# Optimization experiments

Hardware: AMD Instinct MI355X
Metric: run time of the kernel (lower is better)

Reference implementation:

```python
import jax, jax.numpy as jnp
import numpy as np

B, N, C_IN = 8, 2048, 2


def _pdist(x):
    # (B,N,N) pairwise euclidean distances
    d2 = jnp.sum((x[:, :, None, :] - x[:, None, :, :]) ** 2, axis=-1)
    return jnp.sqrt(d2)


def _knn_idx(x, k):
    d = _pdist(x)
    return jnp.argsort(d, axis=-1)[:, :, :k]  # includes self (dist 0)


def _ball_idx(x, radius, nsample):
    # deterministic ball query: neighbors with dist<=radius in ascending index
    # order, cyclically repeated if fewer than nsample (self is always in ball)
    d = _pdist(x)
    n = x.shape[1]
    mask = d <= radius
    ar = jnp.arange(n)
    order = jnp.argsort(jnp.where(mask, ar, ar + n), axis=-1)  # valid idx first
    count = jnp.sum(mask, axis=-1, keepdims=True)               # >= 1
    pos = jnp.arange(nsample)[None, None, :] % count            # (B,N,nsample)
    return jnp.take_along_axis(order, pos, axis=-1)


def _gather(x, idx):
    # x: (B,N,C), idx: (B,N,S) -> (B,N,S,C)
    return jax.vmap(lambda pts, ind: pts[ind])(x, idx)


def _mlp2(f, w0, b0, w1, b1):
    # 1x1 Conv2D stack == per-neighbor dense + relu
    f = jnp.maximum(jnp.einsum('bnsc,cd->bnsd', f, w0) + b0, 0.0)
    f = jnp.maximum(jnp.einsum('bnsc,cd->bnsd', f, w1) + b1, 0.0)
    return f


def _dense_relu(x, w, b):
    return jnp.maximum(x @ w + b, 0.0)


def _forward(x,
             sa1_w0, sa1_b0, sa1_w1, sa1_b1,
             sa2_w0, sa2_b0, sa2_w1, sa2_b1,
             sa3_w0, sa3_b0, sa3_w1, sa3_b1,
             fp1_w0, fp1_b0, fp1_w1, fp1_b1,
             fp2_w0, fp2_b0, fp2_w1, fp2_b1,
             fc1_w, fc1_b, fc2_w, fc2_b, out_w, out_b):
    # SA1: knn(k=32) on raw points, mlps [64,64], mean over neighbors
    x1 = jnp.mean(_mlp2(_gather(x, _knn_idx(x, 32)), sa1_w0, sa1_b0, sa1_w1, sa1_b1), axis=2)
    # SA2: ball query radius=0.2, nsample=32, mlps [128,128]
    x2 = jnp.mean(_mlp2(_gather(x1, _ball_idx(x1, 0.2, 32)), sa2_w0, sa2_b0, sa2_w1, sa2_b1), axis=2)
    # SA3: ball query radius=0.4, nsample=64, mlps [256,256]
    x3 = jnp.mean(_mlp2(_gather(x2, _ball_idx(x2, 0.4, 64)), sa3_w0, sa3_b0, sa3_w1, sa3_b1), axis=2)
    # FP1: dense mlps on local (x2), concat global (x3)
    h = _dense_relu(_dense_relu(x2, fp1_w0, fp1_b0), fp1_w1, fp1_b1)
    h = jnp.concatenate([h, x3], axis=-1)
    # FP2: dense mlps on local (x1), concat previous
    g = _dense_relu(_dense_relu(x1, fp2_w0, fp2_b0), fp2_w1, fp2_b1)
    g = jnp.concatenate([g, h], axis=-1)
    g = _dense_relu(g, fc1_w, fc1_b)
    g = _dense_relu(g, fc2_w, fc2_b)
    return jax.nn.sigmoid(g @ out_w + out_b)  # (B,N,1)


def setup_inputs() -> dict:
    key = jax.random.key(0)
    ks = iter(jax.random.split(key, 40))
    def w(i, o):
        return (jax.random.normal(next(ks), (i, o), jnp.float32) / np.sqrt(i)).astype(jnp.float32)
    def b(o):
        return jnp.zeros((o,), jnp.float32)
    inp = {
        'x': jax.random.normal(next(ks), (B, N, C_IN), jnp.float32),
        'sa1_w0': w(2, 64),   'sa1_b0': b(64),  'sa1_w1': w(64, 64),   'sa1_b1': b(64),
        'sa2_w0': w(64, 128), 'sa2_b0': b(128), 'sa2_w1': w(128, 128), 'sa2_b1': b(128),
        'sa3_w0': w(128, 256),'sa3_b0': b(256), 'sa3_w1': w(256, 256), 'sa3_b1': b(256),
        'fp1_w0': w(128, 512),'fp1_b0': b(512), 'fp1_w1': w(512, 512), 'fp1_b1': b(512),
        'fp2_w0': w(64, 256), 'fp2_b0': b(256), 'fp2_w1': w(256, 256), 'fp2_b1': b(256),
        'fc1_w': w(1024, 256),'fc1_b': b(256),
        'fc2_w': w(256, 128), 'fc2_b': b(128),
        'out_w': w(128, 1),   'out_b': b(1),
    }
    return inp


def reference(x,
              sa1_w0, sa1_b0, sa1_w1, sa1_b1,
              sa2_w0, sa2_b0, sa2_w1, sa2_b1,
              sa3_w0, sa3_b0, sa3_w1, sa3_b1,
              fp1_w0, fp1_b0, fp1_w1, fp1_b1,
              fp2_w0, fp2_b0, fp2_w1, fp2_b1,
              fc1_w, fc1_b, fc2_w, fc2_b, out_w, out_b):
    return _forward(x,
                    sa1_w0, sa1_b0, sa1_w1, sa1_b1,
                    sa2_w0, sa2_b0, sa2_w1, sa2_b1,
                    sa3_w0, sa3_b0, sa3_w1, sa3_b1,
                    fp1_w0, fp1_b0, fp1_w1, fp1_b1,
                    fp2_w0, fp2_b0, fp2_w1, fp2_b1,
                    fc1_w, fc1_b, fc2_w, fc2_b, out_w, out_b)
```

## Files before the change

### kernel.cpp

```cpp
#include <hip/hip_runtime.h>
#include <hip/hip_bf16.h>
#include <cstdint>

#define M_ROWS 16384

typedef __attribute__((ext_vector_type(8))) short short8;
typedef __attribute__((ext_vector_type(4))) float f32x4;

__device__ __forceinline__ unsigned long long umin64(unsigned long long a,
                                                     unsigned long long b) {
  return a < b ? a : b;
}

__global__ __launch_bounds__(256) void gemm_bias_relu(
    const float* __restrict__ X, int ldx,
    const float* __restrict__ W,
    const float* __restrict__ bias,
    float* __restrict__ Y, int ldy,
    int N, int K)
{
  __shared__ __align__(16) float As[16][68];
  __shared__ __align__(16) float Bs[16][68];
  int tid = threadIdx.x;
  int tx = tid & 15, ty = tid >> 4;
  int m0 = blockIdx.y << 6, n0 = blockIdx.x << 6;
  float acc[4][4] = {};
  for (int k0 = 0; k0 < K; k0 += 16) {
#pragma unroll
    for (int i = 0; i < 4; i++) {
      int idx = tid + (i << 8);
      int m = idx >> 4, k = idx & 15;
      As[k][m] = (k0 + k < K) ? X[(size_t)(m0 + m) * ldx + k0 + k] : 0.f;
    }
#pragma unroll
    for (int i = 0; i < 4; i++) {
      int idx = tid + (i << 8);
      int n = idx & 63, k = idx >> 6;
      Bs[k][n] = (k0 + k < K) ? W[(size_t)(k0 + k) * N + n0 + n] : 0.f;
    }
    __syncthreads();
#pragma unroll
    for (int k = 0; k < 16; k++) {
      float4 a4 = *(const float4*)&As[k][ty << 2];
      float4 b4 = *(const float4*)&Bs[k][tx << 2];
      float av[4] = {a4.x, a4.y, a4.z, a4.w};
      float bv[4] = {b4.x, b4.y, b4.z, b4.w};
#pragma unroll
      for (int i = 0; i < 4; i++)
#pragma unroll
        for (int j = 0; j < 4; j++)
          acc[i][j] += av[i] * bv[j];
    }
    __syncthreads();
  }
  float4 bb = *(const float4*)&bias[n0 + (tx << 2)];
  float bv[4] = {bb.x, bb.y, bb.z, bb.w};
#pragma unroll
  for (int i = 0; i < 4; i++) {
    int m = m0 + (ty << 2) + i;
    float4 o;
    o.x = fmaxf(acc[i][0] + bv[0], 0.f);
    o.y = fmaxf(acc[i][1] + bv[1], 0.f);
    o.z = fmaxf(acc[i][2] + bv[2], 0.f);
    o.w = fmaxf(acc[i][3] + bv[3], 0.f);
    *(float4*)&Y[(size_t)m * ldy + n0 + (tx << 2)] = o;
  }
}

struct TJobs {
  const float* W[8];
  __hip_bfloat16* Wt[8];
  int K[8], N[8], bx[8], off[8];
};

__global__ __launch_bounds__(256) void transpose_cast_all(TJobs jb)
{
  __shared__ float tile[32][33];
  int bid = blockIdx.x;
  int j = 0;
#pragma unroll
  for (int t = 1; t < 8; t++)
    if (bid >= jb.off[t]) j = t;
  int rel = bid - jb.off[j];
  int K = jb.K[j], N = jb.N[j];
  const float* W = jb.W[j];
  __hip_bfloat16* Wt = jb.Wt[j];
  int n0 = (rel % jb.bx[j]) << 5, k0 = (rel / jb.bx[j]) << 5;
  int c = threadIdx.x & 31, i0 = threadIdx.x >> 5;
#pragma unroll
  for (int p = 0; p < 4; p++) {
    int i = i0 + p * 8;
    tile[i][c] = W[(size_t)(k0 + i) * N + n0 + c];
  }
  __syncthreads();
#pragma unroll
  for (int p = 0; p < 4; p++) {
    int r = i0 + p * 8;
    Wt[(size_t)(n0 + r) * K + k0 + c] = (__hip_bfloat16)tile[c][r];
  }
}

template <bool OUT_BF16>
__global__ __launch_bounds__(256) void gemm_mfma(
    const __hip_bfloat16* __restrict__ A, int lda,
    const __hip_bfloat16* __restrict__ Wt, int ldw,
    const float* __restrict__ bias,
    void* __restrict__ Y, int ldy, int N, int K)
{
  __shared__ __align__(16) short As[128][40];
  __shared__ __align__(16) short Bs[128][40];
  int tid = threadIdx.x;
  int wave = tid >> 6, lane = tid & 63;
  int quad = lane >> 4, l16 = lane & 15;
  int m0 = blockIdx.y << 7, n0 = blockIdx.x << 7;
  int wm = (wave >> 1) << 6, wn = (wave & 1) << 6;
  f32x4 acc[4][4] = {};
  const short* Ag = (const short*)A;
  const short* Bg = (const short*)Wt;
  int srow = tid >> 2, sq = tid & 3;
  for (int k0 = 0; k0 < K; k0 += 32) {
#pragma unroll
    for (int h = 0; h < 2; h++) {
      int r = srow + (h << 6);
      uint4 va = *(const uint4*)&Ag[(size_t)(m0 + r) * lda + k0 + sq * 8];
      *(uint4*)&As[r][sq * 8] = va;
      uint4 vb = *(const uint4*)&Bg[(size_t)(n0 + r) * ldw + k0 + sq * 8];
      *(uint4*)&Bs[r][sq * 8] = vb;
    }
    __syncthreads();
    short8 a[4], b[4];
#pragma unroll
    for (int mi = 0; mi < 4; mi++)
      a[mi] = *(const short8*)&As[wm + mi * 16 + l16][quad * 8];
#pragma unroll
    for (int ni = 0; ni < 4; ni++)
      b[ni] = *(const short8*)&Bs[wn + ni * 16 + l16][quad * 8];
#pragma unroll
    for (int mi = 0; mi < 4; mi++)
#pragma unroll
      for (int ni = 0; ni < 4; ni++)
        acc[mi][ni] = __builtin_amdgcn_mfma_f32_16x16x32_bf16(
            a[mi], b[ni], acc[mi][ni], 0, 0, 0);
    __syncthreads();
  }
  float bn[4];
#pragma unroll
  for (int ni = 0; ni < 4; ni++) bn[ni] = bias[n0 + wn + ni * 16 + l16];
#pragma unroll
  for (int mi = 0; mi < 4; mi++)
#pragma unroll
    for (int ni = 0; ni < 4; ni++) {
      int n = n0 + wn + ni * 16 + l16;
#pragma unroll
      for (int r = 0; r < 4; r++) {
        int m = m0 + wm + mi * 16 + quad * 4 + r;
        float v = fmaxf(acc[mi][ni][r] + bn[ni], 0.f);
        if (OUT_BF16)
          ((__hip_bfloat16*)Y)[(size_t)m * ldy + n] = (__hip_bfloat16)v;
        else
          ((float*)Y)[(size_t)m * ldy + n] = v;
      }
    }
}

struct GJobs {
  const short* A[3];
  const short* W[3];
  const float* bias[3];
  __hip_bfloat16* Y[3];
  int lda[3], ldw[3], ldy[3], N[3], K[3], xt[3], off[3];
};

__global__ __launch_bounds__(256) void gemm_mfma_multi(GJobs g)
{
  __shared__ __align__(16) short As[128][40];
  __shared__ __align__(16) short Bs[128][40];
  int bid = blockIdx.x;
  int j = 0;
#pragma unroll
  for (int t = 1; t < 3; t++)
    if (bid >= g.off[t]) j = t;
  int rel = bid - g.off[j];
  int xt = g.xt[j];
  int m0 = (rel / xt) << 7, n0 = (rel % xt) << 7;
  int lda = g.lda[j], ldw = g.ldw[j], ldy = g.ldy[j], K = g.K[j];
  const short* Ag = g.A[j];
  const short* Bg = g.W[j];
  const float* bias = g.bias[j];
  __hip_bfloat16* Y = g.Y[j];

  int tid = threadIdx.x;
  int wave = tid >> 6, lane = tid & 63;
  int quad = lane >> 4, l16 = lane & 15;
  int wm = (wave >> 1) << 6, wn = (wave & 1) << 6;
  f32x4 acc[4][4] = {};
  int srow = tid >> 2, sq = tid & 3;
  for (int k0 = 0; k0 < K; k0 += 32) {
#pragma unroll
    for (int h = 0; h < 2; h++) {
      int r = srow + (h << 6);
      uint4 va = *(const uint4*)&Ag[(size_t)(m0 + r) * lda + k0 + sq * 8];
      *(uint4*)&As[r][sq * 8] = va;
      uint4 vb = *(const uint4*)&Bg[(size_t)(n0 + r) * ldw + k0 + sq * 8];
      *(uint4*)&Bs[r][sq * 8] = vb;
    }
    __syncthreads();
    short8 a[4], b[4];
#pragma unroll
    for (int mi = 0; mi < 4; mi++)
      a[mi] = *(const short8*)&As[wm + mi * 16 + l16][quad * 8];
#pragma unroll
    for (int ni = 0; ni < 4; ni++)
      b[ni] = *(const short8*)&Bs[wn + ni * 16 + l16][quad * 8];
#pragma unroll
    for (int mi = 0; mi < 4; mi++)
#pragma unroll
      for (int ni = 0; ni < 4; ni++)
        acc[mi][ni] = __builtin_amdgcn_mfma_f32_16x16x32_bf16(
            a[mi], b[ni], acc[mi][ni], 0, 0, 0);
    __syncthreads();
  }
  float bn[4];
#pragma unroll
  for (int ni = 0; ni < 4; ni++) bn[ni] = bias[n0 + wn + ni * 16 + l16];
#pragma unroll
  for (int mi = 0; mi < 4; mi++)
#pragma unroll
    for (int ni = 0; ni < 4; ni++) {
      int n = n0 + wn + ni * 16 + l16;
#pragma unroll
      for (int r = 0; r < 4; r++) {
        int m = m0 + wm + mi * 16 + quad * 4 + r;
        float v = fmaxf(acc[mi][ni][r] + bn[ni], 0.f);
        Y[(size_t)m * ldy + n] = (__hip_bfloat16)v;
      }
    }
}

__global__ __launch_bounds__(256) void gemm_fc2_out(
    const __hip_bfloat16* __restrict__ A,
    const __hip_bfloat16* __restrict__ Wt,
    const float* __restrict__ bias,
    const float* __restrict__ wout,
    const float* __restrict__ bout,
    float* __restrict__ out)
{
  __shared__ __align__(16) short As[128][40];
  __shared__ __align__(16) short Bs[128][40];
  __shared__ float red[128][2];
  const int N = 128, K = 256, lda = 256, ldw = 256;
  int tid = threadIdx.x;
  int wave = tid >> 6, lane = tid & 63;
  int quad = lane >> 4, l16 = lane & 15;
  int m0 = blockIdx.y << 7;
  int wm = (wave >> 1) << 6, wn = (wave & 1) << 6;
  f32x4 acc[4][4] = {};
  const short* Ag = (const short*)A;
  const short* Bg = (const short*)Wt;
  int srow = tid >> 2, sq = tid & 3;
  for (int k0 = 0; k0 < K; k0 += 32) {
#pragma unroll
    for (int h = 0; h < 2; h++) {
      int r = srow + (h << 6);
      uint4 va = *(const uint4*)&Ag[(size_t)(m0 + r) * lda + k0 + sq * 8];
      *(uint4*)&As[r][sq * 8] = va;
      uint4 vb = *(const uint4*)&Bg[(size_t)(r % N) * ldw + k0 + sq * 8];
      *(uint4*)&Bs[r][sq * 8] = vb;
    }
    __syncthreads();
    short8 a[4], b[4];
#pragma unroll
    for (int mi = 0; mi < 4; mi++)
      a[mi] = *(const short8*)&As[wm + mi * 16 + l16][quad * 8];
#pragma unroll
    for (int ni = 0; ni < 4; ni++)
      b[ni] = *(const short8*)&Bs[wn + ni * 16 + l16][quad * 8];
#pragma unroll
    for (int mi = 0; mi < 4; mi++)
#pragma unroll
      for (int ni = 0; ni < 4; ni++)
        acc[mi][ni] = __builtin_amdgcn_mfma_f32_16x16x32_bf16(
            a[mi], b[ni], acc[mi][ni], 0, 0, 0);
    __syncthreads();
  }
  float bn[4], wo[4];
#pragma unroll
  for (int ni = 0; ni < 4; ni++) {
    int n = wn + ni * 16 + l16;
    bn[ni] = bias[n];
    wo[ni] = wout[n];
  }
  float sacc[4][4];
#pragma unroll
  for (int mi = 0; mi < 4; mi++)
#pragma unroll
    for (int r = 0; r < 4; r++) {
      float s = 0.f;
#pragma unroll
      for (int ni = 0; ni < 4; ni++)
        s += fmaxf(acc[mi][ni][r] + bn[ni], 0.f) * wo[ni];
      sacc[mi][r] = s;
    }
#pragma unroll
  for (int off = 1; off < 16; off <<= 1)
#pragma unroll
    for (int mi = 0; mi < 4; mi++)
#pragma unroll
      for (int r = 0; r < 4; r++)
        sacc[mi][r] += __shfl_xor(sacc[mi][r], off);
  int wp = wave & 1;
  if (l16 == 0) {
#pragma unroll
    for (int mi = 0; mi < 4; mi++)
#pragma unroll
      for (int r = 0; r < 4; r++)
        red[wm + mi * 16 + quad * 4 + r][wp] = sacc[mi][r];
  }
  __syncthreads();
  if (tid < 128) {
    float s = red[tid][0] + red[tid][1] + bout[0];
    out[(size_t)(m0 + tid)] = 1.f / (1.f + expf(-s));
  }
}

__global__ __launch_bounds__(256) void knn_mean_kernel(
    const float* __restrict__ X,
    const float* __restrict__ G1,
    float* __restrict__ X1,
    __hip_bfloat16* __restrict__ X1b,
    __hip_bfloat16* __restrict__ X1lo,
    float* __restrict__ nrmX1)
{
  int q = blockIdx.x;
  int base = q & ~2047;
  int tid = threadIdx.x;
  __shared__ unsigned long long lmins[256];
  __shared__ unsigned long long qmins[64];
  __shared__ unsigned long long surv[2048];
  __shared__ unsigned long long thr;
  __shared__ int scnt;
  __shared__ int selidx[32];
  if (tid == 0) scnt = 0;
  float qx = X[(size_t)q * 2], qy = X[(size_t)q * 2 + 1];
  unsigned long long key[8];
#pragma unroll
  for (int u = 0; u < 8; u++) {
    int j = (u << 8) + tid;
    float dx = X[(size_t)(base + j) * 2] - qx;
    float dy = X[(size_t)(base + j) * 2 + 1] - qy;
    float d2 = dx * dx + dy * dy;
    key[u] = ((unsigned long long)__float_as_uint(d2) << 32) | (unsigned)j;
  }
  unsigned long long lm = key[0];
#pragma unroll
  for (int u = 1; u < 8; u++) lm = umin64(lm, key[u]);
  lmins[tid] = lm;
  __syncthreads();
  if (tid < 64) {
    unsigned long long qm = umin64(umin64(lmins[tid], lmins[tid + 64]),
                                   umin64(lmins[tid + 128], lmins[tid + 192]));
    qmins[tid] = qm;
    int rank = 0;
    for (int i = 0; i < 64; i++) rank += (qmins[i] < qm);
    if (rank == 31) thr = qm;
  }
  __syncthreads();
  unsigned long long T = thr;
#pragma unroll
  for (int u = 0; u < 8; u++) {
    if (key[u] <= T) {
      int p = atomicAdd(&scnt, 1);
      surv[p] = key[u];
    }
  }
  __syncthreads();
  int s = scnt;
  for (int i = tid; i < s; i += 256) {
    unsigned long long c = surv[i];
    int r = 0;
    for (int j2 = 0; j2 < s; j2++) r += (surv[j2] < c);
    if (r < 32) selidx[r] = (int)(c & 0xffffffffULL);
  }
  __syncthreads();
  if (tid < 64) {
    float acc = 0.f;
#pragma unroll 4
    for (int sI = 0; sI < 32; sI++)
      acc += G1[(size_t)(base + selidx[sI]) * 64 + tid];
    float v = acc * (1.0f / 32.0f);
    X1[(size_t)q * 64 + tid] = v;
    __hip_bfloat16 hi = (__hip_bfloat16)v;
    X1b[(size_t)q * 64 + tid] = hi;
    X1lo[(size_t)q * 64 + tid] = (__hip_bfloat16)(v - (float)hi);
    float nv = v * v;
#pragma unroll
    for (int off = 32; off > 0; off >>= 1) nv += __shfl_down(nv, off);
    if (tid == 0) nrmX1[q] = nv;
  }
}

template <int C>
__global__ __launch_bounds__(256) void ball_mask_mfma(
    const float* __restrict__ F32,
    const __hip_bfloat16* __restrict__ Fhi,
    const __hip_bfloat16* __restrict__ Flo,
    const float* __restrict__ nrm,
    unsigned long long* __restrict__ mask,
    float r2)
{
  __shared__ __align__(16) short Qh[128][40];
  __shared__ __align__(16) short Ql[128][40];
  __shared__ __align__(16) short Ch[128][40];
  __shared__ __align__(16) short Cl[128][40];
  __shared__ unsigned int tw[128][4];
  __shared__ float nqs[128], ncs[128];
  int tid = threadIdx.x;
  int p = blockIdx.x;
  int qt = 0;
  while (p >= 16 - qt) { p -= 16 - qt; qt++; }
  int ct = qt + p;
  int b0 = blockIdx.y << 11;
  int q0 = b0 + (qt << 7), c0 = b0 + (ct << 7);
  tw[tid >> 1][(tid & 1) * 2] = 0;
  tw[tid >> 1][(tid & 1) * 2 + 1] = 0;
  if (tid < 128) nqs[tid] = nrm[q0 + tid];
  else ncs[tid - 128] = nrm[c0 + tid - 128];

  int wave = tid >> 6, lane = tid & 63;
  int quad = lane >> 4, l16 = lane & 15;
  int wm = (wave >> 1) << 6, wn = (wave & 1) << 6;
  f32x4 acc[4][4] = {};
  const short* QH = (const short*)Fhi;
  const short* QL = (const short*)Flo;
  int srow = tid >> 2, sq = tid & 3;
  for (int k0 = 0; k0 < C; k0 += 32) {
#pragma unroll
    for (int h = 0; h < 2; h++) {
      int r = srow + (h << 6);
      *(uint4*)&Qh[r][sq * 8] = *(const uint4*)&QH[(size_t)(q0 + r) * C + k0 + sq * 8];
      *(uint4*)&Ql[r][sq * 8] = *(const uint4*)&QL[(size_t)(q0 + r) * C + k0 + sq * 8];
      *(uint4*)&Ch[r][sq * 8] = *(const uint4*)&QH[(size_t)(c0 + r) * C + k0 + sq * 8];
      *(uint4*)&Cl[r][sq * 8] = *(const uint4*)&QL[(size_t)(c0 + r) * C + k0 + sq * 8];
    }
    __syncthreads();
    short8 ah[4], al[4];
#pragma unroll
    for (int mi = 0; mi < 4; mi++) {
      ah[mi] = *(const short8*)&Qh[wm + mi * 16 + l16][quad * 8];
      al[mi] = *(const short8*)&Ql[wm + mi * 16 + l16][quad * 8];
    }
#pragma unroll
    for (int ni = 0; ni < 4; ni++) {
      short8 bh = *(const short8*)&Ch[wn + ni * 16 + l16][quad * 8];
      short8 bl = *(const short8*)&Cl[wn + ni * 16 + l16][quad * 8];
#pragma unroll
      for (int mi = 0; mi < 4; mi++) {
        acc[mi][ni] = __builtin_amdgcn_mfma_f32_16x16x32_bf16(ah[mi], bh, acc[mi][ni], 0, 0, 0);
        acc[mi][ni] = __builtin_amdgcn_mfma_f32_16x16x32_bf16(ah[mi], bl, acc[mi][ni], 0, 0, 0);
        acc[mi][ni] = __builtin_amdgcn_mfma_f32_16x16x32_bf16(al[mi], bh, acc[mi][ni], 0, 0, 0);
      }
    }
    __syncthreads();
  }
  unsigned long long memb = 0, fb = 0;
#pragma unroll
  for (int mi = 0; mi < 4; mi++)
#pragma unroll
    for (int ni = 0; ni < 4; ni++)
#pragma unroll
      for (int r = 0; r < 4; r++) {
        int e = (mi << 4) | (ni << 2) | r;
        float nqv = nqs[wm + mi * 16 + quad * 4 + r];
        float ncv = ncs[wn + ni * 16 + l16];
        float d2a = nqv + ncv - 2.f * acc[mi][ni][r];
        float eps = 4.0e-5f * (nqv + ncv) + 1.0e-6f;
        if (d2a < r2 - eps) memb |= 1ull << e;
        else if (d2a <= r2 + eps) fb |= 1ull << e;
      }
  while (fb) {
    int e = __builtin_ctzll(fb);
    fb &= fb - 1;
    int mi = e >> 4, ni = (e >> 2) & 3, r = e & 3;
    int qrow = q0 + wm + mi * 16 + quad * 4 + r;
    int ccol = c0 + wn + ni * 16 + l16;
    float a2 = 0.f;
    for (int k = 0; k < C; k++) {
      float d = F32[(size_t)qrow * C + k] - F32[(size_t)ccol * C + k];
      a2 = fmaf(d, d, a2);
    }
    if (a2 <= r2) memb |= 1ull << e;
  }
#pragma unroll
  for (int ni = 0; ni < 4; ni++) {
    int cl = wn + ni * 16 + l16;
    unsigned int w0b = 0, w1b = 0;
#pragma unroll
    for (int mi = 0; mi < 4; mi++)
#pragma unroll
      for (int r = 0; r < 4; r++)
        if (memb & (1ull << ((mi << 4) | (ni << 2) | r))) {
          unsigned int bitpos = ((mi & 1) << 4) | (quad << 2) | r;
          if (mi < 2) w0b |= 1u << bitpos;
          else w1b |= 1u << bitpos;
        }
    if (w0b) atomicOr(&tw[cl][(wm >> 5)], w0b);
    if (w1b) atomicOr(&tw[cl][(wm >> 5) + 1], w1b);
  }
  __syncthreads();
  {
    int row = tid >> 1, half = tid & 1;
    int wq = row >> 5, sb = row & 31;
    unsigned int lo = 0, hi = 0;
    for (int j = 0; j < 32; j++) {
      lo |= ((tw[half * 64 + j][wq] >> sb) & 1u) << j;
      hi |= ((tw[half * 64 + 32 + j][wq] >> sb) & 1u) << j;
    }
    mask[(size_t)(q0 + row) * 32 + (ct << 1) + half] =
        ((unsigned long long)hi << 32) | lo;
  }
  if (qt != ct) {
    int row = tid >> 1, word = tid & 1;
    unsigned long long v = (unsigned long long)tw[row][word * 2] |
                           ((unsigned long long)tw[row][word * 2 + 1] << 32);
    mask[(size_t)(c0 + row) * 32 + (qt << 1) + word] = v;
  }
}

template <typename TIn>
__global__ void ball_gather_kernel(
    const unsigned long long* __restrict__ mask,
    const TIn* __restrict__ H, int CH,
    float* __restrict__ Yf, __hip_bfloat16* __restrict__ Yb,
    __hip_bfloat16* __restrict__ Ylo, float* __restrict__ nrm,
    int ldy, int S)
{
  int q = blockIdx.x;
  int base = q & ~2047;
  int tid = threadIdx.x;
  __shared__ int idxl[64];
  __shared__ float wtab[64];
  __shared__ float npart[4];
  __shared__ int scount;
  if (tid < 32) {
    unsigned long long w = mask[(size_t)q * 32 + tid];
    int cnt = __popcll(w);
    int inc = cnt;
#pragma unroll
    for (int off = 1; off < 32; off <<= 1) {
      int o = __shfl_up(inc, off);
      if (tid >= off) inc += o;
    }
    if (tid == 31) scount = inc;
    int p = inc - cnt;
    while (w && p < 64) {
      int j = (tid << 6) + __builtin_ctzll(w);
      w &= w - 1;
      idxl[p++] = j;
    }
  }
  __syncthreads();
  int c = scount;
  if (tid < 64) {
    int p = tid;
    int cnt = (p < c && p < S) ? ((S - 1 - p) / c + 1) : 0;
    wtab[p] = (float)cnt / (float)S;
  }
  __syncthreads();
  float acc = 0.f;
  int lim = c < S ? c : S;
#pragma unroll 4
  for (int s = 0; s < lim; s++)
    acc += wtab[s] * (float)H[(size_t)(base + idxl[s]) * CH + tid];
  if (Yf) Yf[(size_t)q * ldy + tid] = acc;
  if (Yb) Yb[(size_t)q * ldy + tid] = (__hip_bfloat16)acc;
  if (Ylo) {
    __hip_bfloat16 hi = (__hip_bfloat16)acc;
    Ylo[(size_t)q * ldy + tid] = (__hip_bfloat16)(acc - (float)hi);
  }
  if (nrm) {
    float nv = acc * acc;
#pragma unroll
    for (int off = 32; off > 0; off >>= 1) nv += __shfl_down(nv, off);
    if ((tid & 63) == 0) npart[tid >> 6] = nv;
    __syncthreads();
    if (tid == 0) {
      float t = 0.f;
      for (int w = 0; w < (blockDim.x >> 6); w++) t += npart[w];
      nrm[q] = t;
    }
  }
}

extern "C" void kernel_launch(void* const* d_in, const int* in_sizes, int n_in,
                              void* d_out, int out_size, void* d_ws,
                              size_t ws_size, hipStream_t stream)
{
  const float* x      = (const float*)d_in[0];
  const float* sa1_w0 = (const float*)d_in[1];
  const float* sa1_b0 = (const float*)d_in[2];
  const float* sa1_w1 = (const float*)d_in[3];
  const float* sa1_b1 = (const float*)d_in[4];
  const float* sa2_w0 = (const float*)d_in[5];
  const float* sa2_b0 = (const float*)d_in[6];
  const float* sa2_w1 = (const float*)d_in[7];
  const float* sa2_b1 = (const float*)d_in[8];
  const float* sa3_w0 = (const float*)d_in[9];
  const float* sa3_b0 = (const float*)d_in[10];
  const float* sa3_w1 = (const float*)d_in[11];
  const float* sa3_b1 = (const float*)d_in[12];
  const float* fp1_w0 = (const float*)d_in[13];
  const float* fp1_b0 = (const float*)d_in[14];
  const float* fp1_w1 = (const float*)d_in[15];
  const float* fp1_b1 = (const float*)d_in[16];
  const float* fp2_w0 = (const float*)d_in[17];
  const float* fp2_b0 = (const float*)d_in[18];
  const float* fp2_w1 = (const float*)d_in[19];
  const float* fp2_b1 = (const float*)d_in[20];
  const float* fc1_w  = (const float*)d_in[21];
  const float* fc1_b  = (const float*)d_in[22];
  const float* fc2_w  = (const float*)d_in[23];
  const float* fc2_b  = (const float*)d_in[24];
  const float* out_w  = (const float*)d_in[25];
  const float* out_b  = (const float*)d_in[26];
  float* out = (float*)d_out;

  const size_t M = M_ROWS;
  float* ws = (float*)d_ws;
  float* T   = ws;
  float* G1  = ws + M * 256;
  float* X1  = ws + M * 320;
  float* X2  = ws + M * 384;
  float* H2  = ws + M * 512;
  __hip_bfloat16* H3b16 = (__hip_bfloat16*)(ws + M * 640);
  unsigned long long* MASK = (unsigned long long*)(ws + M * 896);
  __hip_bfloat16* X1b = (__hip_bfloat16*)(ws + M * 960);
  __hip_bfloat16* X2b = (__hip_bfloat16*)(ws + M * 992);
  __hip_bfloat16* TB0 = (__hip_bfloat16*)(ws + M * 1056);
  __hip_bfloat16* TB1 = (__hip_bfloat16*)(ws + M * 1184);
  __hip_bfloat16* TB2 = (__hip_bfloat16*)(ws + M * 1440);
  __hip_bfloat16* G   = (__hip_bfloat16*)(ws + M * 1568);
  __hip_bfloat16* H3b = (__hip_bfloat16*)(ws + M * 2080);
  __hip_bfloat16* WB  = (__hip_bfloat16*)(ws + M * 2208);
  __hip_bfloat16* X1lo = (__hip_bfloat16*)(ws + M * 2240);
  __hip_bfloat16* X2lo = (__hip_bfloat16*)(ws + M * 2272);
  float* nrmX1 = ws + M * 2336;
  float* nrmX2 = ws + M * 2337;
  if (ws_size < (size_t)M * 2340 * sizeof(float)) return;
  __hip_bfloat16* w_sa3_0 = WB;
  __hip_bfloat16* w_sa3_1 = w_sa3_0 + 32768;
  __hip_bfloat16* w_fp1_0 = w_sa3_1 + 65536;
  __hip_bfloat16* w_fp1_1 = w_fp1_0 + 65536;
  __hip_bfloat16* w_fp2_0 = w_fp1_1 + 262144;
  __hip_bfloat16* w_fp2_1 = w_fp2_0 + 16384;
  __hip_bfloat16* w_fc1   = w_fp2_1 + 65536;
  __hip_bfloat16* w_fc2   = w_fc1 + 262144;

  dim3 blk(256);
  TJobs jb;
  const float* srcs[8] = {sa3_w0, sa3_w1, fp1_w0, fp1_w1, fp2_w0, fp2_w1, fc1_w, fc2_w};
  __hip_bfloat16* dsts[8] = {w_sa3_0, w_sa3_1, w_fp1_0, w_fp1_1, w_fp2_0, w_fp2_1, w_fc1, w_fc2};
  int Ks[8] = {128, 256, 128, 512, 64, 256, 1024, 256};
  int Ns[8] = {256, 256, 512, 512, 256, 256, 256, 128};
  int off = 0;
  for (int i = 0; i < 8; i++) {
    jb.W[i] = srcs[i]; jb.Wt[i] = dsts[i];
    jb.K[i] = Ks[i]; jb.N[i] = Ns[i];
    jb.bx[i] = Ns[i] >> 5;
    jb.off[i] = off;
    off += (Ns[i] >> 5) * (Ks[i] >> 5);
  }
  transpose_cast_all<<<off, blk, 0, stream>>>(jb);

  gemm_bias_relu<<<dim3(1, 256), blk, 0, stream>>>(x, 2, sa1_w0, sa1_b0, T, 64, 64, 2);
  gemm_bias_relu<<<dim3(1, 256), blk, 0, stream>>>(T, 64, sa1_w1, sa1_b1, G1, 64, 64, 64);
  knn_mean_kernel<<<16384, 256, 0, stream>>>(x, G1, X1, X1b, X1lo, nrmX1);
  gemm_bias_relu<<<dim3(2, 256), blk, 0, stream>>>(X1, 64, sa2_w0, sa2_b0, T, 128, 128, 64);
  gemm_bias_relu<<<dim3(2, 256), blk, 0, stream>>>(T, 128, sa2_w1, sa2_b1, H2, 128, 128, 128);
  ball_mask_mfma<64><<<dim3(136, 8), blk, 0, stream>>>(X1, X1b, X1lo, nrmX1, MASK, 0.2f * 0.2f);
  ball_gather_kernel<float><<<16384, 128, 0, stream>>>(MASK, H2, 128, X2, X2b, X2lo, nrmX2, 128, 32);
  ball_mask_mfma<128><<<dim3(136, 8), blk, 0, stream>>>(X2, X2b, X2lo, nrmX2, MASK, 0.4f * 0.4f);
  {
    GJobs g1;
    g1.A[0] = (const short*)X2b; g1.W[0] = (const short*)w_sa3_0; g1.bias[0] = sa3_b0;
    g1.Y[0] = TB0; g1.lda[0] = 128; g1.ldw[0] = 128; g1.ldy[0] = 256; g1.N[0] = 256; g1.K[0] = 128;
    g1.A[1] = (const short*)X2b; g1.W[1] = (const short*)w_fp1_0; g1.bias[1] = fp1_b0;
    g1.Y[1] = TB1; g1.lda[1] = 128; g1.ldw[1] = 128; g1.ldy[1] = 512; g1.N[1] = 512; g1.K[1] = 128;
    g1.A[2] = (const short*)X1b; g1.W[2] = (const short*)w_fp2_0; g1.bias[2] = fp2_b0;
    g1.Y[2] = TB2; g1.lda[2] = 64; g1.ldw[2] = 64; g1.ldy[2] = 256; g1.N[2] = 256; g1.K[2] = 64;
    int tot1 = 0;
    for (int i = 0; i < 3; i++) {
      g1.xt[i] = g1.N[i] >> 7;
      g1.off[i] = tot1;
      tot1 += g1.xt[i] * 128;
    }
    gemm_mfma_multi<<<tot1, blk, 0, stream>>>(g1);

    GJobs g2;
    g2.A[0] = (const short*)TB0; g2.W[0] = (const short*)w_sa3_1; g2.bias[0] = sa3_b1;
    g2.Y[0] = H3b16; g2.lda[0] = 256; g2.ldw[0] = 256; g2.ldy[0] = 256; g2.N[0] = 256; g2.K[0] = 256;
    g2.A[1] = (const short*)TB1; g2.W[1] = (const short*)w_fp1_1; g2.bias[1] = fp1_b1;
    g2.Y[1] = G + 256; g2.lda[1] = 512; g2.ldw[1] = 512; g2.ldy[1] = 1024; g2.N[1] = 512; g2.K[1] = 512;
    g2.A[2] = (const short*)TB2; g2.W[2] = (const short*)w_fp2_1; g2.bias[2] = fp2_b1;
    g2.Y[2] = G; g2.lda[2] = 256; g2.ldw[2] = 256; g2.ldy[2] = 1024; g2.N[2] = 256; g2.K[2] = 256;
    int tot2 = 0;
    for (int i = 0; i < 3; i++) {
      g2.xt[i] = g2.N[i] >> 7;
      g2.off[i] = tot2;
      tot2 += g2.xt[i] * 128;
    }
    gemm_mfma_multi<<<tot2, blk, 0, stream>>>(g2);
  }
  ball_gather_kernel<__hip_bfloat16><<<16384, 256, 0, stream>>>(
      MASK, H3b16, 256, nullptr, G + 768, nullptr, nullptr, 1024, 64);
  gemm_mfma<true><<<dim3(2, 128), blk, 0, stream>>>(G, 1024, w_fc1, 1024, fc1_b, H3b, 256, 256, 1024);
  gemm_fc2_out<<<dim3(1, 128), blk, 0, stream>>>(H3b, w_fc2, fc2_b, out_w, out_b, out);
}
```

Baseline: 402.6 us.

## Process four kNN queries per block to reuse candidate coordinate loads

```diff
diff --git a/kernel.cpp b/kernel.cpp
--- a/kernel.cpp
+++ b/kernel.cpp
@@ -323,7 +323,7 @@
   }
 }
 
-__global__ __launch_bounds__(256) void knn_mean_kernel(
+__global__ __launch_bounds__(256) void knn_mean4(
     const float* __restrict__ X,
     const float* __restrict__ G1,
     float* __restrict__ X1,
@@ -331,71 +331,90 @@
     __hip_bfloat16* __restrict__ X1lo,
     float* __restrict__ nrmX1)
 {
-  int q = blockIdx.x;
-  int base = q & ~2047;
+  int qb = blockIdx.x << 2;
+  int base = qb & ~2047;
   int tid = threadIdx.x;
-  __shared__ unsigned long long lmins[256];
-  __shared__ unsigned long long qmins[64];
+  int wave = tid >> 6, lane = tid & 63;
+  __shared__ unsigned long long lmins[4][256];
+  __shared__ unsigned long long qmins[4][64];
+  __shared__ unsigned long long thr[4];
   __shared__ unsigned long long surv[2048];
-  __shared__ unsigned long long thr;
   __shared__ int scnt;
-  __shared__ int selidx[32];
-  if (tid == 0) scnt = 0;
-  float qx = X[(size_t)q * 2], qy = X[(size_t)q * 2 + 1];
-  unsigned long long key[8];
+  __shared__ int selidx[4][32];
+  float xj[8], yj[8];
 #pragma unroll
   for (int u = 0; u < 8; u++) {
     int j = (u << 8) + tid;
-    float dx = X[(size_t)(base + j) * 2] - qx;
-    float dy = X[(size_t)(base + j) * 2 + 1] - qy;
-    float d2 = dx * dx + dy * dy;
-    key[u] = ((unsigned long long)__float_as_uint(d2) << 32) | (unsigned)j;
-  }
-  unsigned long long lm = key[0];
-#pragma unroll
-  for (int u = 1; u < 8; u++) lm = umin64(lm, key[u]);
-  lmins[tid] = lm;
+    float2 c = *(const float2*)&X[(size_t)(base + j) * 2];
+    xj[u] = c.x;
+    yj[u] = c.y;
+  }
+  unsigned long long key[4][8];
+#pragma unroll
+  for (int g = 0; g < 4; g++) {
+    float qx = X[(size_t)(qb + g) * 2];
+    float qy = X[(size_t)(qb + g) * 2 + 1];
+    unsigned long long lm = ~0ull;
+#pragma unroll
+    for (int u = 0; u < 8; u++) {
+      float dx = xj[u] - qx;
+      float dy = yj[u] - qy;
+      float d2 = dx * dx + dy * dy;
+      key[g][u] = ((unsigned long long)__float_as_uint(d2) << 32) |
+                  (unsigned)((u << 8) + tid);
+      lm = umin64(lm, key[g][u]);
+    }
+    lmins[g][tid] = lm;
+  }
   __syncthreads();
-  if (tid < 64) {
-    unsigned long long qm = umin64(umin64(lmins[tid], lmins[tid + 64]),
-                                   umin64(lmins[tid + 128], lmins[tid + 192]));
-    qmins[tid] = qm;
+  {
+    int g = wave;
+    unsigned long long qm =
+        umin64(umin64(lmins[g][lane], lmins[g][lane + 64]),
+               umin64(lmins[g][lane + 128], lmins[g][lane + 192]));
+    qmins[g][lane] = qm;
     int rank = 0;
-    for (int i = 0; i < 64; i++) rank += (qmins[i] < qm);
-    if (rank == 31) thr = qm;
+    for (int i = 0; i < 64; i++) rank += (qmins[g][i] < qm);
+    if (rank == 31) thr[g] = qm;
   }
   __syncthreads();
-  unsigned long long T = thr;
-#pragma unroll
-  for (int u = 0; u < 8; u++) {
-    if (key[u] <= T) {
-      int p = atomicAdd(&scnt, 1);
-      surv[p] = key[u];
-    }
-  }
-  __syncthreads();
-  int s = scnt;
-  for (int i = tid; i < s; i += 256) {
-    unsigned long long c = surv[i];
-    int r = 0;
-    for (int j2 = 0; j2 < s; j2++) r += (surv[j2] < c);
-    if (r < 32) selidx[r] = (int)(c & 0xffffffffULL);
-  }
-  __syncthreads();
-  if (tid < 64) {
+  for (int g = 0; g < 4; g++) {
+    if (tid == 0) scnt = 0;
+    __syncthreads();
+    unsigned long long T = thr[g];
+#pragma unroll
+    for (int u = 0; u < 8; u++) {
+      if (key[g][u] <= T) {
+        int p = atomicAdd(&scnt, 1);
+        surv[p] = key[g][u];
+      }
+    }
+    __syncthreads();
+    int s = scnt;
+    for (int i = tid; i < s; i += 256) {
+      unsigned long long c = surv[i];
+      int r = 0;
+      for (int j2 = 0; j2 < s; j2++) r += (surv[j2] < c);
+      if (r < 32) selidx[g][r] = (int)(c & 0xffffffffULL);
+    }
+    __syncthreads();
+  }
+  {
+    int g = wave;
     float acc = 0.f;
 #pragma unroll 4
     for (int sI = 0; sI < 32; sI++)
-      acc += G1[(size_t)(base + selidx[sI]) * 64 + tid];
+      acc += G1[(size_t)(base + selidx[g][sI]) * 64 + lane];
     float v = acc * (1.0f / 32.0f);
-    X1[(size_t)q * 64 + tid] = v;
+    int q = qb + g;
+    X1[(size_t)q * 64 + lane] = v;
     __hip_bfloat16 hi = (__hip_bfloat16)v;
-    X1b[(size_t)q * 64 + tid] = hi;
-    X1lo[(size_t)q * 64 + tid] = (__hip_bfloat16)(v - (float)hi);
+    X1b[(size_t)q * 64 + lane] = hi;
+    X1lo[(size_t)q * 64 + lane] = (__hip_bfloat16)(v - (float)hi);
     float nv = v * v;
 #pragma unroll
     for (int off = 32; off > 0; off >>= 1) nv += __shfl_down(nv, off);
-    if (tid == 0) nrmX1[q] = nv;
+    if (lane == 0) nrmX1[q] = nv;
   }
 }
 
@@ -568,7 +587,7 @@
   __syncthreads();
   float acc = 0.f;
   int lim = c < S ? c : S;
-#pragma unroll 4
+#pragma unroll 8
   for (int s = 0; s < lim; s++)
     acc += wtab[s] * (float)H[(size_t)(base + idxl[s]) * CH + tid];
   if (Yf) Yf[(size_t)q * ldy + tid] = acc;
@@ -673,7 +692,7 @@
 
   gemm_bias_relu<<<dim3(1, 256), blk, 0, stream>>>(x, 2, sa1_w0, sa1_b0, T, 64, 64, 2);
   gemm_bias_relu<<<dim3(1, 256), blk, 0, stream>>>(T, 64, sa1_w1, sa1_b1, G1, 64, 64, 64);
-  knn_mean_kernel<<<16384, 256, 0, stream>>>(x, G1, X1, X1b, X1lo, nrmX1);
+  knn_mean4<<<4096, 256, 0, stream>>>(x, G1, X1, X1b, X1lo, nrmX1);
   gemm_bias_relu<<<dim3(2, 256), blk, 0, stream>>>(X1, 64, sa2_w0, sa2_b0, T, 128, 128, 64);
   gemm_bias_relu<<<dim3(2, 256), blk, 0, stream>>>(T, 128, sa2_w1, sa2_b1, H2, 128, 128, 128);
   ball_mask_mfma<64><<<dim3(136, 8), blk, 0, stream>>>(X1, X1b, X1lo, nrmX1, MASK, 0.2f * 0.2f);
```

Result: faster. 391.1 us (-2.9%).
